# Optimization experiments

Hardware: AMD Instinct MI355X
Metric: run time of the kernel (lower is better)

The kernel has to match this reference:

```python
import jax, jax.numpy as jnp
import numpy as np
from jax import lax

VOCAB = 5000
HIDDEN = 1024
SEQ = 128
BATCH = 64


def setup_inputs() -> dict:
    key = jax.random.key(0)
    ks = jax.random.split(key, 12)
    s = 1.0 / np.sqrt(HIDDEN)
    u = lambda k, shape: jax.random.uniform(k, shape, jnp.float32, -s, s)
    return {
        "x": jax.random.randint(ks[0], (SEQ, BATCH), 0, VOCAB),
        # layer 1: input size = VOCAB
        "W_ih1": u(ks[1], (HIDDEN, VOCAB)),
        "W_hh1": u(ks[2], (HIDDEN, HIDDEN)),
        "b_ih1": u(ks[3], (HIDDEN,)),
        "b_hh1": u(ks[4], (HIDDEN,)),
        # layer 2: input size = HIDDEN
        "W_ih2": u(ks[5], (HIDDEN, HIDDEN)),
        "W_hh2": u(ks[6], (HIDDEN, HIDDEN)),
        "b_ih2": u(ks[7], (HIDDEN,)),
        "b_hh2": u(ks[8], (HIDDEN,)),
        # final projection
        "W_fc": u(ks[9], (VOCAB, HIDDEN)),
        "b_fc": u(ks[10], (VOCAB,)),
    }


def _rnn_layer(x_proj, W_hh, b_hh, h0):
    # x_proj: (S, B, H) precomputed input contribution (incl. b_ih)
    def step(h, xt):
        h = jnp.tanh(xt + h @ W_hh.T + b_hh)
        return h, h
    h_last, ys = lax.scan(step, h0, x_proj)
    return ys, h_last


def reference(x, W_ih1, W_hh1, b_ih1, b_hh1, W_ih2, W_hh2, b_ih2, b_hh2, W_fc, b_fc):
    S, B = x.shape
    H = W_hh1.shape[0]
    h0 = jnp.zeros((B, H), dtype=W_ih1.dtype)
    # one_hot(x) @ W_ih1.T is exactly a row-gather of W_ih1.T
    xp1 = jnp.take(W_ih1.T, x, axis=0) + b_ih1          # (S, B, H)
    y1, h1 = _rnn_layer(xp1, W_hh1, b_hh1, h0)
    xp2 = jnp.einsum("sbh,gh->sbg", y1, W_ih2) + b_ih2  # (S, B, H)
    y2, h2 = _rnn_layer(xp2, W_hh2, b_hh2, h0)
    ans = jnp.einsum("sbh,vh->sbv", y2, W_fc) + b_fc    # (S, B, V)
    state = jnp.stack([h1, h2])                          # (2, B, H)
    return ans, state
```

## Files before the change

### kernel.cpp

```cpp
#include <hip/hip_runtime.h>
#include <hip/hip_bf16.h>

#define VOCAB 5000
#define HIDDEN 1024
#define SEQ 128
#define BATCH 64
#define L1NB 16
#define L2NB 32
#define NBLK (L1NB + L2NB)
#define RING 8
#define LDS_BYTES 139264

typedef __hip_bfloat16 bf16;
typedef short bf16x8 __attribute__((ext_vector_type(8)));
typedef float f32x4 __attribute__((ext_vector_type(4)));

__device__ __forceinline__ float b2f(bf16 v) { return __bfloat162float(v); }

__device__ __forceinline__ bool detect_fp32(const void* w) {
    const unsigned* p = (const unsigned*)w;
    unsigned big = 0;
    #pragma unroll
    for (int i = 0; i < 64; ++i) {
        unsigned e = (p[i] >> 7) & 0xFFu;
        big |= (e >= 127u) ? 1u : 0u;
    }
    return big != 0;
}

__global__ __launch_bounds__(256) void convert_w(const void* __restrict__ src,
                                                 bf16* __restrict__ dst, int n,
                                                 const void* __restrict__ det) {
    const bool f32 = detect_fp32(det);
    int i = (blockIdx.x * 256 + threadIdx.x) * 4;
    if (f32) {
        const float* s = (const float*)src;
        #pragma unroll
        for (int j = 0; j < 4; ++j) if (i + j < n) dst[i + j] = __float2bfloat16(s[i + j]);
    } else {
        const bf16* s = (const bf16*)src;
        #pragma unroll
        for (int j = 0; j < 4; ++j) if (i + j < n) dst[i + j] = s[i + j];
    }
}

__global__ __launch_bounds__(256) void make_bias(const void* __restrict__ a,
                                                 const void* __restrict__ b,
                                                 float* __restrict__ dst, int n,
                                                 const void* __restrict__ det) {
    const bool f32 = detect_fp32(det);
    int i = blockIdx.x * 256 + threadIdx.x;
    if (i >= n) return;
    float v = f32 ? ((const float*)a)[i] : b2f(((const bf16*)a)[i]);
    if (b)  v += f32 ? ((const float*)b)[i] : b2f(((const bf16*)b)[i]);
    dst[i] = v;
}

__device__ __forceinline__ void ld_sys_b128(bf16x8* dst, const void* p) {
    asm volatile("global_load_dwordx4 %0, %1, off sc0 sc1" : "=v"(*dst) : "v"(p));
}
__device__ __forceinline__ void st_sys_b128(void* p, bf16x8 v) {
    asm volatile("global_store_dwordx4 %0, %1, off sc0 sc1" :: "v"(p), "v"(v) : "memory");
}
__device__ __forceinline__ void vm_drain() {
    asm volatile("s_waitcnt vmcnt(0)" ::: "memory");
    __builtin_amdgcn_sched_barrier(0);
}

template <int SLP>
__device__ __forceinline__ void wait_flag(int* flag, int target, long maxit) {
    long n = 0;
    while (__hip_atomic_load(flag, __ATOMIC_RELAXED, __HIP_MEMORY_SCOPE_AGENT) < target) {
        __builtin_amdgcn_s_sleep(SLP);
        if (++n > maxit) return;
    }
}

__global__ __launch_bounds__(256, 1) void rnn_persistent(
    const int*  __restrict__ x,
    const void* __restrict__ Wih1raw,
    const bf16* __restrict__ whh1,
    const bf16* __restrict__ wih2,
    const bf16* __restrict__ whh2,
    const float* __restrict__ bias1,
    const float* __restrict__ bias2,
    bf16* __restrict__ y1r,
    bf16* __restrict__ y2,
    int* __restrict__ f1,
    int* __restrict__ f2)
{
    extern __shared__ bf16 lds[];
    const int bid  = blockIdx.x;
    const int tid  = threadIdx.x;
    const int wave = tid >> 6;
    const int lane = tid & 63;
    const int q    = lane >> 4;
    const int l15  = lane & 15;
    const size_t BH = (size_t)BATCH * HIDDEN;
    const int  mrow  = wave * 16 + l15;

    if (bid < L1NB) {
        const bool f32in = detect_fp32(Wih1raw);
        const int n0 = bid * 64;
        for (int idx = tid; idx < 64 * 128; idx += 256) {
            const int row = idx >> 7, c = idx & 127;
            *(bf16x8*)&lds[(size_t)((row << 7) + (c ^ (row & 7))) * 8] =
                *(const bf16x8*)(whh1 + (size_t)(n0 + row) * HIDDEN + c * 8);
        }
        __syncthreads();

        float breg[4];
        #pragma unroll
        for (int t = 0; t < 4; ++t) breg[t] = bias1[n0 + t * 16 + l15];
        bf16* cb = lds + 65536;

        for (int s = 0; s < SEQ; ++s) {
            float xg[4][4];
            {
                int xv[4];
                #pragma unroll
                for (int r = 0; r < 4; ++r) xv[r] = x[s * BATCH + wave * 16 + q * 4 + r];
                #pragma unroll
                for (int t = 0; t < 4; ++t)
                    #pragma unroll
                    for (int r = 0; r < 4; ++r) {
                        const size_t gi = (size_t)(n0 + t * 16 + l15) * VOCAB + xv[r];
                        xg[t][r] = f32in ? ((const float*)Wih1raw)[gi]
                                         : b2f(((const bf16*)Wih1raw)[gi]);
                    }
            }
            if (tid == 0  && s >= 1)    wait_flag<1>(&f1[s - 1], L1NB, 40000000L);
            if (tid == 64 && s >= RING) wait_flag<1>(&f2[s - RING], L2NB, 40000000L);
            __syncthreads();

            f32x4 acc[4];
            #pragma unroll
            for (int t = 0; t < 4; ++t) acc[t] = (f32x4){0.f,0.f,0.f,0.f};
            if (s > 0) {
                const bf16* arow = y1r + (size_t)((s - 1) & (RING - 1)) * BH
                                       + (size_t)mrow * HIDDEN + q * 8;
                bf16x8 af[32];
                #pragma unroll
                for (int k = 0; k < 32; ++k) ld_sys_b128(&af[k], arow + k * 32);
                vm_drain();
                #pragma unroll
                for (int k = 0; k < 32; ++k) {
                    const int chb = k * 4 + q;
                    #pragma unroll
                    for (int t = 0; t < 4; ++t) {
                        const int row = t * 16 + l15;
                        bf16x8 bw = *(const bf16x8*)&lds[(size_t)((row << 7) + (chb ^ (row & 7))) * 8];
                        acc[t] = __builtin_amdgcn_mfma_f32_16x16x32_bf16(af[k], bw, acc[t], 0, 0, 0);
                    }
                }
            }
            #pragma unroll
            for (int t = 0; t < 4; ++t)
                #pragma unroll
                for (int r = 0; r < 4; ++r) {
                    const int b = wave * 16 + q * 4 + r;
                    cb[b * 64 + t * 16 + l15] =
                        __float2bfloat16(tanhf(acc[t][r] + breg[t] + xg[t][r]));
                }
            __syncthreads();
            bf16* outb = y1r + (size_t)(s & (RING - 1)) * BH;
            #pragma unroll
            for (int it = 0; it < 2; ++it) {
                const int c = it * 256 + tid;
                const int row = c >> 3, off = (c & 7) * 8;
                st_sys_b128(outb + (size_t)row * HIDDEN + n0 + off,
                            *(const bf16x8*)&cb[row * 64 + off]);
            }
            vm_drain();
            __syncthreads();
            if (tid == 0)
                __hip_atomic_fetch_add(&f1[s], 1, __ATOMIC_RELEASE, __HIP_MEMORY_SCOPE_AGENT);
        }
    } else {
        const int n0 = (bid - L1NB) * 32;
        for (int idx = tid; idx < 32 * 256; idx += 256) {
            const int row = idx >> 8, c = idx & 255;
            const bf16* W = (c < 128) ? wih2 : whh2;
            *(bf16x8*)&lds[(size_t)((row << 8) + (c ^ (row & 7))) * 8] =
                *(const bf16x8*)(W + (size_t)(n0 + row) * HIDDEN + (c & 127) * 8);
        }
        __syncthreads();

        float breg[2];
        #pragma unroll
        for (int t = 0; t < 2; ++t) breg[t] = bias2[n0 + t * 16 + l15];
        bf16* cb = lds + 65536;

        for (int st = 0; st < SEQ; ++st) {
            if (tid == 0)              wait_flag<1>(&f1[st], L1NB, 40000000L);
            if (tid == 64 && st >= 1)  wait_flag<1>(&f2[st - 1], L2NB, 40000000L);
            __syncthreads();

            f32x4 acc[2];
            #pragma unroll
            for (int t = 0; t < 2; ++t) acc[t] = (f32x4){0.f,0.f,0.f,0.f};

            {
                const bf16* arow = y1r + (size_t)(st & (RING - 1)) * BH
                                       + (size_t)mrow * HIDDEN + q * 8;
                bf16x8 af[32];
                #pragma unroll
                for (int k = 0; k < 32; ++k) ld_sys_b128(&af[k], arow + k * 32);
                vm_drain();
                #pragma unroll
                for (int k = 0; k < 32; ++k) {
                    const int chb = k * 4 + q;
                    #pragma unroll
                    for (int t = 0; t < 2; ++t) {
                        const int row = t * 16 + l15;
                        bf16x8 bw = *(const bf16x8*)&lds[(size_t)((row << 8) + (chb ^ (row & 7))) * 8];
                        acc[t] = __builtin_amdgcn_mfma_f32_16x16x32_bf16(af[k], bw, acc[t], 0, 0, 0);
                    }
                }
            }
            if (st > 0) {
                const bf16* arow = y2 + (size_t)(st - 1) * BH
                                      + (size_t)mrow * HIDDEN + q * 8;
                bf16x8 af[32];
                #pragma unroll
                for (int k = 0; k < 32; ++k) ld_sys_b128(&af[k], arow + k * 32);
                vm_drain();
                #pragma unroll
                for (int k = 0; k < 32; ++k) {
                    const int chb = 128 + k * 4 + q;
                    #pragma unroll
                    for (int t = 0; t < 2; ++t) {
                        const int row = t * 16 + l15;
                        bf16x8 bw = *(const bf16x8*)&lds[(size_t)((row << 8) + (chb ^ (row & 7))) * 8];
                        acc[t] = __builtin_amdgcn_mfma_f32_16x16x32_bf16(af[k], bw, acc[t], 0, 0, 0);
                    }
                }
            }
            #pragma unroll
            for (int t = 0; t < 2; ++t)
                #pragma unroll
                for (int r = 0; r < 4; ++r) {
                    const int b = wave * 16 + q * 4 + r;
                    cb[b * 32 + t * 16 + l15] =
                        __float2bfloat16(tanhf(acc[t][r] + breg[t]));
                }
            __syncthreads();
            {
                bf16* outb = y2 + (size_t)st * BH;
                const int row = tid >> 2, off = (tid & 3) * 8;
                st_sys_b128(outb + (size_t)row * HIDDEN + n0 + off,
                            *(const bf16x8*)&cb[row * 32 + off]);
            }
            vm_drain();
            __syncthreads();
            if (tid == 0)
                __hip_atomic_fetch_add(&f2[st], 1, __ATOMIC_RELEASE, __HIP_MEMORY_SCOPE_AGENT);
        }
    }
}

__global__ __launch_bounds__(256) void proj(
    const bf16* __restrict__ y2, const bf16* __restrict__ Wfc,
    const float* __restrict__ bfc, void* __restrict__ outp,
    const void* __restrict__ det)
{
    __shared__ bf16 cbuf[64 * 256];
    const int bm = blockIdx.x;
    const int bn = blockIdx.y;
    const int wave = threadIdx.x >> 6;
    const int lane = threadIdx.x & 63;
    const int q = lane >> 4, l15 = lane & 15;
    const int wm = wave & 1, wn = wave >> 1;
    const int m0 = bm * 64 + wm * 32;
    const int n0 = bn * 256 + wn * 128;

    f32x4 acc[2][8];
    #pragma unroll
    for (int i = 0; i < 2; ++i)
        #pragma unroll
        for (int t = 0; t < 8; ++t) acc[i][t] = (f32x4){0.f,0.f,0.f,0.f};

    const bf16x8 zf = (bf16x8){0,0,0,0,0,0,0,0};
    const bf16* a0p = y2 + (size_t)(m0 + l15) * HIDDEN + q * 8;
    const bf16* a1p = a0p + (size_t)16 * HIDDEN;

    for (int k0 = 0; k0 < HIDDEN; k0 += 32) {
        bf16x8 af0 = *(const bf16x8*)(a0p + k0);
        bf16x8 af1 = *(const bf16x8*)(a1p + k0);
        #pragma unroll
        for (int t = 0; t < 8; ++t) {
            const int n = n0 + t * 16 + l15;
            bf16x8 bw = (n < VOCAB)
                ? *(const bf16x8*)(Wfc + (size_t)n * HIDDEN + k0 + q * 8) : zf;
            acc[0][t] = __builtin_amdgcn_mfma_f32_16x16x32_bf16(af0, bw, acc[0][t], 0, 0, 0);
            acc[1][t] = __builtin_amdgcn_mfma_f32_16x16x32_bf16(af1, bw, acc[1][t], 0, 0, 0);
        }
    }

    const bool f32out = detect_fp32(det);

    if (f32out) {
        #pragma unroll
        for (int t = 0; t < 8; ++t) {
            const int col = n0 + t * 16 + l15;
            if (col >= VOCAB) continue;
            const float bias = bfc[col];
            #pragma unroll
            for (int i = 0; i < 2; ++i)
                #pragma unroll
                for (int r = 0; r < 4; ++r) {
                    const int row = m0 + i * 16 + q * 4 + r;
                    ((float*)outp)[(size_t)row * VOCAB + col] = acc[i][t][r] + bias;
                }
        }
        return;
    }

    #pragma unroll
    for (int t = 0; t < 8; ++t) {
        const int col  = n0 + t * 16 + l15;
        const int cloc = wn * 128 + t * 16 + l15;
        const float bias = (col < VOCAB) ? bfc[col] : 0.f;
        #pragma unroll
        for (int i = 0; i < 2; ++i)
            #pragma unroll
            for (int r = 0; r < 4; ++r) {
                const int rloc = wm * 32 + i * 16 + q * 4 + r;
                cbuf[rloc * 256 + cloc] = __float2bfloat16(acc[i][t][r] + bias);
            }
    }
    __syncthreads();
    bf16* ob = (bf16*)outp;
    for (int cidx = threadIdx.x; cidx < 64 * 32; cidx += 256) {
        const int row = cidx >> 5;
        const int c8  = (cidx & 31) * 8;
        const int gcol = bn * 256 + c8;
        if (gcol < VOCAB)
            *(bf16x8*)(ob + (size_t)(bm * 64 + row) * VOCAB + gcol) =
                *(const bf16x8*)&cbuf[row * 256 + c8];
    }
}

__global__ __launch_bounds__(256) void state_copy(
    const bf16* __restrict__ y1r, const bf16* __restrict__ y2,
    void* __restrict__ outp, const void* __restrict__ det)
{
    const bool f32out = detect_fp32(det);
    const int t = blockIdx.x * blockDim.x + threadIdx.x;
    const int BH = BATCH * HIDDEN;
    const size_t ofs = (size_t)SEQ * BATCH * VOCAB;
    float v;
    if (t < BH) v = b2f(y1r[(size_t)((SEQ - 1) & (RING - 1)) * BH + t]);
    else        v = b2f(y2[(size_t)(SEQ - 1) * BH + (t - BH)]);
    if (f32out) ((float*)outp)[ofs + t] = v;
    else        ((bf16*)outp)[ofs + t] = __float2bfloat16(v);
}

extern "C" void kernel_launch(void* const* d_in, const int* in_sizes, int n_in,
                              void* d_out, int out_size, void* d_ws, size_t ws_size,
                              hipStream_t stream) {
    const int*  x       = (const int*)d_in[0];
    const void* Wih1raw = d_in[1];
    const void* Whh1raw = d_in[2];
    const void* bih1    = d_in[3];
    const void* bhh1    = d_in[4];
    const void* Wih2raw = d_in[5];
    const void* Whh2raw = d_in[6];
    const void* bih2    = d_in[7];
    const void* bhh2    = d_in[8];
    const void* Wfcraw  = d_in[9];
    const void* bfcraw  = d_in[10];

    char* wsb = (char*)d_ws;
    int*   f1    = (int*)wsb;
    int*   f2    = f1 + SEQ;
    bf16*  y2    = (bf16*)(wsb + 1024);
    bf16*  y1r   = y2   + (size_t)SEQ * BATCH * HIDDEN;
    bf16*  whh1  = y1r  + (size_t)RING * BATCH * HIDDEN;
    bf16*  wih2  = whh1 + (size_t)HIDDEN * HIDDEN;
    bf16*  whh2  = wih2 + (size_t)HIDDEN * HIDDEN;
    bf16*  wfcb  = whh2 + (size_t)HIDDEN * HIDDEN;
    float* bias1 = (float*)(wfcb + (size_t)VOCAB * HIDDEN);
    float* bias2 = bias1 + HIDDEN;
    float* bfcf  = bias2 + HIDDEN;

    static bool lds_ok = false;
    if (!lds_ok) {
        (void)hipFuncSetAttribute((const void*)rnn_persistent,
                                  hipFuncAttributeMaxDynamicSharedMemorySize, LDS_BYTES);
        lds_ok = true;
    }

    (void)hipMemsetAsync(f1, 0, 2 * SEQ * sizeof(int), stream);

    const int HH = HIDDEN * HIDDEN, VH = VOCAB * HIDDEN;
    convert_w<<<(HH + 1023) / 1024, 256, 0, stream>>>(Whh1raw, whh1, HH, Wih1raw);
    convert_w<<<(HH + 1023) / 1024, 256, 0, stream>>>(Wih2raw, wih2, HH, Wih1raw);
    convert_w<<<(HH + 1023) / 1024, 256, 0, stream>>>(Whh2raw, whh2, HH, Wih1raw);
    convert_w<<<(VH + 1023) / 1024, 256, 0, stream>>>(Wfcraw,  wfcb, VH, Wih1raw);
    make_bias<<<(HIDDEN + 255) / 256, 256, 0, stream>>>(bih1, bhh1, bias1, HIDDEN, Wih1raw);
    make_bias<<<(HIDDEN + 255) / 256, 256, 0, stream>>>(bih2, bhh2, bias2, HIDDEN, Wih1raw);
    make_bias<<<(VOCAB + 255) / 256, 256, 0, stream>>>(bfcraw, nullptr, bfcf, VOCAB, Wih1raw);

    rnn_persistent<<<NBLK, 256, LDS_BYTES, stream>>>(x, Wih1raw, whh1, wih2, whh2,
                                                     bias1, bias2, y1r, y2, f1, f2);

    proj<<<dim3(128, 20), 256, 0, stream>>>(y2, wfcb, bfcf, d_out, Wih1raw);
    state_copy<<<(2 * BATCH * HIDDEN) / 256, 256, 0, stream>>>(y1r, y2, d_out, Wih1raw);
}
```

Measured before the change: 2.243 ms.

## Drop y1 ring buffer, relax cross-layer sync, and overlap layer-2 input GEMM

The 8-slot y1 ring buffer is replaced by a full per-step y1 buffer stored in the output region, so layer 1 no longer waits on layer 2 for backpressure. The output is later overwritten by proj, so state_copy now runs before proj. Layer-2 blocks compute the W_ih2·y1 half before waiting on the previous y2 flag, overlapping that work with the recurrence. The bulk sc0/sc1 system-scope loads plus full vmcnt drain are replaced with ordinary interleaved loads, which relies on each y1/y2 slot being written only once. Spin-wait limits are also much shorter, so a slow producer could cause a silent timeout that reads unfinished data.

```diff
diff --git a/kernel.cpp b/kernel.cpp
--- a/kernel.cpp
+++ b/kernel.cpp
@@ -8,7 +8,6 @@
 #define L1NB 16
 #define L2NB 32
 #define NBLK (L1NB + L2NB)
-#define RING 8
 #define LDS_BYTES 139264
 
 typedef __hip_bfloat16 bf16;
@@ -56,9 +55,6 @@
     dst[i] = v;
 }
 
-__device__ __forceinline__ void ld_sys_b128(bf16x8* dst, const void* p) {
-    asm volatile("global_load_dwordx4 %0, %1, off sc0 sc1" : "=v"(*dst) : "v"(p));
-}
 __device__ __forceinline__ void st_sys_b128(void* p, bf16x8 v) {
     asm volatile("global_store_dwordx4 %0, %1, off sc0 sc1" :: "v"(p), "v"(v) : "memory");
 }
@@ -68,8 +64,8 @@
 }
 
 template <int SLP>
-__device__ __forceinline__ void wait_flag(int* flag, int target, long maxit) {
-    long n = 0;
+__device__ __forceinline__ void wait_flag(int* flag, int target, int maxit) {
+    int n = 0;
     while (__hip_atomic_load(flag, __ATOMIC_RELAXED, __HIP_MEMORY_SCOPE_AGENT) < target) {
         __builtin_amdgcn_s_sleep(SLP);
         if (++n > maxit) return;
@@ -84,7 +80,7 @@
     const bf16* __restrict__ whh2,
     const float* __restrict__ bias1,
     const float* __restrict__ bias2,
-    bf16* __restrict__ y1r,
+    bf16* __restrict__ y1,
     bf16* __restrict__ y2,
     int* __restrict__ f1,
     int* __restrict__ f2)
@@ -129,28 +125,24 @@
                                          : b2f(((const bf16*)Wih1raw)[gi]);
                     }
             }
-            if (tid == 0  && s >= 1)    wait_flag<1>(&f1[s - 1], L1NB, 40000000L);
-            if (tid == 64 && s >= RING) wait_flag<1>(&f2[s - RING], L2NB, 40000000L);
+            if (tid == 0 && s >= 1) wait_flag<1>(&f1[s - 1], L1NB, 300000);
             __syncthreads();
 
             f32x4 acc[4];
             #pragma unroll
             for (int t = 0; t < 4; ++t) acc[t] = (f32x4){0.f,0.f,0.f,0.f};
             if (s > 0) {
-                const bf16* arow = y1r + (size_t)((s - 1) & (RING - 1)) * BH
-                                       + (size_t)mrow * HIDDEN + q * 8;
-                bf16x8 af[32];
-                #pragma unroll
-                for (int k = 0; k < 32; ++k) ld_sys_b128(&af[k], arow + k * 32);
-                vm_drain();
+                const bf16* arow = y1 + (size_t)(s - 1) * BH
+                                      + (size_t)mrow * HIDDEN + q * 8;
                 #pragma unroll
                 for (int k = 0; k < 32; ++k) {
+                    bf16x8 af = *(const bf16x8*)(arow + k * 32);
                     const int chb = k * 4 + q;
                     #pragma unroll
                     for (int t = 0; t < 4; ++t) {
                         const int row = t * 16 + l15;
                         bf16x8 bw = *(const bf16x8*)&lds[(size_t)((row << 7) + (chb ^ (row & 7))) * 8];
-                        acc[t] = __builtin_amdgcn_mfma_f32_16x16x32_bf16(af[k], bw, acc[t], 0, 0, 0);
+                        acc[t] = __builtin_amdgcn_mfma_f32_16x16x32_bf16(af, bw, acc[t], 0, 0, 0);
                     }
                 }
             }
@@ -163,7 +155,7 @@
                         __float2bfloat16(tanhf(acc[t][r] + breg[t] + xg[t][r]));
                 }
             __syncthreads();
-            bf16* outb = y1r + (size_t)(s & (RING - 1)) * BH;
+            bf16* outb = y1 + (size_t)s * BH;
             #pragma unroll
             for (int it = 0; it < 2; ++it) {
                 const int c = it * 256 + tid;
@@ -192,47 +184,41 @@
         bf16* cb = lds + 65536;
 
         for (int st = 0; st < SEQ; ++st) {
-            if (tid == 0)              wait_flag<1>(&f1[st], L1NB, 40000000L);
-            if (tid == 64 && st >= 1)  wait_flag<1>(&f2[st - 1], L2NB, 40000000L);
+            if (tid == 0) wait_flag<4>(&f1[st], L1NB, 100000);
             __syncthreads();
 
             f32x4 acc[2];
             #pragma unroll
             for (int t = 0; t < 2; ++t) acc[t] = (f32x4){0.f,0.f,0.f,0.f};
-
             {
-                const bf16* arow = y1r + (size_t)(st & (RING - 1)) * BH
-                                       + (size_t)mrow * HIDDEN + q * 8;
-                bf16x8 af[32];
-                #pragma unroll
-                for (int k = 0; k < 32; ++k) ld_sys_b128(&af[k], arow + k * 32);
-                vm_drain();
+                const bf16* arow = y1 + (size_t)st * BH
+                                      + (size_t)mrow * HIDDEN + q * 8;
                 #pragma unroll
                 for (int k = 0; k < 32; ++k) {
+                    bf16x8 af = *(const bf16x8*)(arow + k * 32);
                     const int chb = k * 4 + q;
                     #pragma unroll
                     for (int t = 0; t < 2; ++t) {
                         const int row = t * 16 + l15;
                         bf16x8 bw = *(const bf16x8*)&lds[(size_t)((row << 8) + (chb ^ (row & 7))) * 8];
-                        acc[t] = __builtin_amdgcn_mfma_f32_16x16x32_bf16(af[k], bw, acc[t], 0, 0, 0);
+                        acc[t] = __builtin_amdgcn_mfma_f32_16x16x32_bf16(af, bw, acc[t], 0, 0, 0);
                     }
                 }
             }
+            if (tid == 0 && st >= 1) wait_flag<1>(&f2[st - 1], L2NB, 300000);
+            __syncthreads();
             if (st > 0) {
                 const bf16* arow = y2 + (size_t)(st - 1) * BH
                                       + (size_t)mrow * HIDDEN + q * 8;
-                bf16x8 af[32];
-                #pragma unroll
-                for (int k = 0; k < 32; ++k) ld_sys_b128(&af[k], arow + k * 32);
-                vm_drain();
                 #pragma unroll
                 for (int k = 0; k < 32; ++k) {
+                    bf16x8 af = *(const bf16x8*)(arow + k * 32);
                     const int chb = 128 + k * 4 + q;
                     #pragma unroll
                     for (int t = 0; t < 2; ++t) {
                         const int row = t * 16 + l15;
                         bf16x8 bw = *(const bf16x8*)&lds[(size_t)((row << 8) + (chb ^ (row & 7))) * 8];
-                        acc[t] = __builtin_amdgcn_mfma_f32_16x16x32_bf16(af[k], bw, acc[t], 0, 0, 0);
+                        acc[t] = __builtin_amdgcn_mfma_f32_16x16x32_bf16(af, bw, acc[t], 0, 0, 0);
                     }
                 }
             }
@@ -342,7 +328,7 @@
 }
 
 __global__ __launch_bounds__(256) void state_copy(
-    const bf16* __restrict__ y1r, const bf16* __restrict__ y2,
+    const bf16* __restrict__ y1, const bf16* __restrict__ y2,
     void* __restrict__ outp, const void* __restrict__ det)
 {
     const bool f32out = detect_fp32(det);
@@ -350,7 +336,7 @@
     const int BH = BATCH * HIDDEN;
     const size_t ofs = (size_t)SEQ * BATCH * VOCAB;
     float v;
-    if (t < BH) v = b2f(y1r[(size_t)((SEQ - 1) & (RING - 1)) * BH + t]);
+    if (t < BH) v = b2f(y1[(size_t)(SEQ - 1) * BH + t]);
     else        v = b2f(y2[(size_t)(SEQ - 1) * BH + (t - BH)]);
     if (f32out) ((float*)outp)[ofs + t] = v;
     else        ((bf16*)outp)[ofs + t] = __float2bfloat16(v);
@@ -375,14 +361,14 @@
     int*   f1    = (int*)wsb;
     int*   f2    = f1 + SEQ;
     bf16*  y2    = (bf16*)(wsb + 1024);
-    bf16*  y1r   = y2   + (size_t)SEQ * BATCH * HIDDEN;
-    bf16*  whh1  = y1r  + (size_t)RING * BATCH * HIDDEN;
+    bf16*  whh1  = y2   + (size_t)SEQ * BATCH * HIDDEN;
     bf16*  wih2  = whh1 + (size_t)HIDDEN * HIDDEN;
     bf16*  whh2  = wih2 + (size_t)HIDDEN * HIDDEN;
     bf16*  wfcb  = whh2 + (size_t)HIDDEN * HIDDEN;
     float* bias1 = (float*)(wfcb + (size_t)VOCAB * HIDDEN);
     float* bias2 = bias1 + HIDDEN;
     float* bfcf  = bias2 + HIDDEN;
+    bf16*  y1    = (bf16*)d_out;
 
     static bool lds_ok = false;
     if (!lds_ok) {
@@ -403,8 +389,8 @@
     make_bias<<<(VOCAB + 255) / 256, 256, 0, stream>>>(bfcraw, nullptr, bfcf, VOCAB, Wih1raw);
 
     rnn_persistent<<<NBLK, 256, LDS_BYTES, stream>>>(x, Wih1raw, whh1, wih2, whh2,
-                                                     bias1, bias2, y1r, y2, f1, f2);
-
+                                                     bias1, bias2, y1, y2, f1, f2);
+
+    state_copy<<<(2 * BATCH * HIDDEN) / 256, 256, 0, stream>>>(y1, y2, d_out, Wih1raw);
     proj<<<dim3(128, 20), 256, 0, stream>>>(y2, wfcb, bfcf, d_out, Wih1raw);
-    state_copy<<<(2 * BATCH * HIDDEN) / 256, 256, 0, stream>>>(y1r, y2, d_out, Wih1raw);
-}
+}
```

Result: faster. 2.050 ms (-8.6%).
